# Kernel tuning notes

Hardware: AMD Instinct MI355X
Metric: run time of the kernel (lower is better)

## Reference

```python
import jax, jax.numpy as jnp
import numpy as np

K_MAX_X = 16
K_MAX_T = 16


def _k_actual(N, k_max):
    # low-mode indices [0..k_max] ++ [N-k_max..N-1], mapped to signed frequencies
    idx = np.concatenate([np.arange(k_max + 1), np.arange(N - k_max, N)]).astype(np.float32)
    return np.where(idx <= (N - 1) // 2, idx, idx - N)


def _phase(N, k_max, sign):
    # separable 1D truncated DFT factor: exp(sign*2*pi*i*k*n/N)/sqrt(N), shape [modes, N]
    k = _k_actual(N, k_max)
    n = np.arange(N, dtype=np.float32)
    ang = sign * 2.0 * np.pi * k[:, None] * n[None, :] / N
    return jnp.asarray((np.exp(1j * ang) / np.sqrt(N)).astype(np.complex64))


def setup_inputs() -> dict:
    key = jax.random.key(0)
    k1, k2, k3 = jax.random.split(key, 3)
    B, C_in, C_out, H, W = 16, 64, 64, 128, 128
    modes = 2 * K_MAX_X + 1  # 33
    scale = 1.0 / (C_in * C_out)
    x = jax.random.normal(k1, (B, C_in, H, W), dtype=jnp.float32)
    wr = scale * jax.random.uniform(k2, (C_in, C_out, modes, modes), dtype=jnp.float32)
    wi = scale * jax.random.uniform(k3, (C_in, C_out, modes, modes), dtype=jnp.float32)
    return {"x": x, "weights_real": wr, "weights_imag": wi}


def reference(x, weights_real, weights_imag):
    B, C, H, W = x.shape
    Px_f = _phase(H, K_MAX_X, -1.0)  # [mx, H]
    Pt_f = _phase(W, K_MAX_T, -1.0)  # [mt, W]
    Px_i = _phase(H, K_MAX_X, +1.0)
    Pt_i = _phase(W, K_MAX_T, +1.0)
    xc = x.astype(jnp.complex64)
    # truncated 2D DFT (separable): X[b,c,i,j]
    X = jnp.einsum('bcnm,in,jm->bcij', xc, Px_f, Pt_f)
    R = (weights_real + 1j * weights_imag).astype(jnp.complex64)
    out_kept = jnp.einsum('bcij,coij->boij', X, R)
    # truncated inverse DFT back to grid
    out = jnp.einsum('boij,in,jm->bonm', out_kept, Px_i, Pt_i)
    return jnp.real(out)
```

## Files before the change

### kernel.cpp

```cpp
#include <hip/hip_runtime.h>


#define NB   16
#define NC   64
#define NO   64
#define NH   128
#define NW   128
#define NM   33
#define WMODE (NM*NM)
#define MPAD  1092
#define NIMG 1024
#define NTOT (64*64*WMODE)
#define CPLANE (64*WMODE)

typedef __attribute__((ext_vector_type(8))) short s8v;
typedef __attribute__((ext_vector_type(4))) float f4v;

__device__ inline unsigned short f2bf(float f) {
  union { float f; unsigned u; } v; v.f = f;
  unsigned r = (v.u + 0x7FFFu + ((v.u >> 16) & 1u)) >> 16;
  return (unsigned short)r;
}

__device__ inline float bflo(unsigned u) {
  union { unsigned u; float f; } cv; cv.u = u << 16; return cv.f;
}
__device__ inline float bfhi(unsigned u) {
  union { unsigned u; float f; } cv; cv.u = u & 0xFFFF0000u; return cv.f;
}

__device__ inline s8v pack8(float4 a, float4 b) {
  s8v r;
  r[0] = (short)f2bf(a.x); r[1] = (short)f2bf(a.y);
  r[2] = (short)f2bf(a.z); r[3] = (short)f2bf(a.w);
  r[4] = (short)f2bf(b.x); r[5] = (short)f2bf(b.y);
  r[6] = (short)f2bf(b.z); r[7] = (short)f2bf(b.w);
  return r;
}

__device__ inline uint2 pack4(f4v a) {
  uint2 p;
  p.x = (unsigned)f2bf(a[0]) | ((unsigned)f2bf(a[1]) << 16);
  p.y = (unsigned)f2bf(a[2]) | ((unsigned)f2bf(a[3]) << 16);
  return p;
}

__device__ inline unsigned short phase_bf(int f, int x) {
  if (f >= 66) return 0;
  int g = (f < 33) ? f : f - 33;
  int fr = (g <= 16) ? g : g + 95;
  int ph = (fr * x) & 127;
  float ang = (float)ph * 0.04908738521234052f;
  float v = ((f < 33) ? cosf(ang) : sinf(ang)) * 0.08838834764831845f;
  return f2bf(v);
}

__global__ __launch_bounds__(256) void spc_tables(short* __restrict__ T1,
                                                  short* __restrict__ T2,
                                                  short* __restrict__ T3,
                                                  short* __restrict__ T4) {
  int tid = blockIdx.x * 256 + threadIdx.x;
  if (tid >= 49152) return;
  int f, x; short* dst;
  if (tid < 10240) {
    int e = tid & 7, l = (tid >> 3) & 63, q = tid >> 9;
    int ks = q / 5, jt = q - 5 * ks;
    f = jt * 16 + (l & 15); x = ks * 32 + (l >> 4) * 8 + e; dst = T1 + tid;
  } else if (tid < 20480) {
    int u = tid - 10240;
    int e = u & 7, l = (u >> 3) & 63, q = u >> 9;
    int it = q >> 2, ks = q & 3;
    f = it * 16 + (l & 15); x = ks * 32 + (l >> 4) * 8 + e; dst = T2 + u;
  } else if (tid < 36864) {
    int u = tid - 20480;
    int e = u & 7, l = (u >> 3) & 63, q = u >> 9;
    int cs = q >> 4, ks = (q >> 3) & 1, mt = q & 7;
    int j = ks * 32 + (l >> 4) * 8 + e;
    f = (j < 33) ? cs * 33 + j : 66;
    x = mt * 16 + (l & 15); dst = T3 + u;
  } else {
    int u = tid - 36864;
    int e = u & 7, l = (u >> 3) & 63, q = u >> 9;
    int nt = q / 3, ks = q - 3 * nt;
    int i2 = ks * 32 + (l >> 4) * 8 + e;
    if (i2 < 48) f = (i2 < 33) ? i2 : 66;
    else         f = (i2 - 48 < 33) ? 33 + (i2 - 48) : 66;
    x = nt * 16 + (l & 15); dst = T4 + u;
  }
  *dst = (short)phase_bf(f, x);
}

__global__ __launch_bounds__(256) void spc_wpack(const float* __restrict__ wr,
                                                 const float* __restrict__ wi,
                                                 unsigned* __restrict__ Wpk) {
  const int t = threadIdx.x;
  const size_t base = (size_t)blockIdx.x * 8192;
#pragma unroll 1
  for (int p = 0; p < 8; ++p) {
    const size_t L = base + (size_t)p * 1024 + (size_t)t * 4;
    if (L + 4 <= (size_t)NTOT) {
      float4 a = *reinterpret_cast<const float4*>(wr + L);
      float4 b = *reinterpret_cast<const float4*>(wi + L);
      float ae[4] = {a.x, a.y, a.z, a.w};
      float be[4] = {b.x, b.y, b.z, b.w};
#pragma unroll
      for (int e = 0; e < 4; ++e) {
        unsigned Li = (unsigned)L + e;
        unsigned c = Li / (unsigned)CPLANE;
        unsigned rem = Li - c * (unsigned)CPLANE;
        unsigned o = rem / (unsigned)WMODE;
        unsigned m = rem - o * (unsigned)WMODE;
        unsigned mch = m >> 6, ml = m & 63u;
        size_t D = ((((size_t)(o >> 1) * 18 + mch) * 64 + c) * 2 + (o & 1)) * 64 + ml;
        Wpk[D] = (unsigned)f2bf(ae[e]) | ((unsigned)f2bf(be[e]) << 16);
      }
    } else {
#pragma unroll
      for (int e = 0; e < 4; ++e) {
        size_t Li = L + e;
        if (Li < (size_t)NTOT) {
          unsigned Lu = (unsigned)Li;
          unsigned c = Lu / (unsigned)CPLANE;
          unsigned rem = Lu - c * (unsigned)CPLANE;
          unsigned o = rem / (unsigned)WMODE;
          unsigned m = rem - o * (unsigned)WMODE;
          unsigned mch = m >> 6, ml = m & 63u;
          size_t D = ((((size_t)(o >> 1) * 18 + mch) * 64 + c) * 2 + (o & 1)) * 64 + ml;
          Wpk[D] = (unsigned)f2bf(wr[Li]) | ((unsigned)f2bf(wi[Li]) << 16);
        }
      }
    }
  }
}

__global__ __launch_bounds__(256) void spc_fwd_mfma(const float* __restrict__ x,
                                                    const s8v* __restrict__ T1,
                                                    const s8v* __restrict__ T2,
                                                    unsigned* __restrict__ X2u) {
  __shared__ short Wt[80 * 128];
  __shared__ float Gs[80 * 84];
  const int t = threadIdx.x;
  const int l = t & 63;
  const int w = t >> 6;
  const int lr = l & 15;
  const int lg = l >> 4;
  const int img = blockIdx.x;
  const float* xp = x + (size_t)img * (NH * NW);

  for (int nn = 0; nn < 2; ++nn) {
    const int nt = 2 * w + nn;
    const float* xrow = xp + (nt * 16 + lr) * NW + lg * 8;
    s8v a[4];
#pragma unroll
    for (int ks = 0; ks < 4; ++ks) {
      float4 f0 = *reinterpret_cast<const float4*>(xrow + ks * 32);
      float4 f1 = *reinterpret_cast<const float4*>(xrow + ks * 32 + 4);
      a[ks] = pack8(f0, f1);
    }
#pragma unroll
    for (int jt = 0; jt < 5; ++jt) {
      f4v acc = {0.f, 0.f, 0.f, 0.f};
#pragma unroll
      for (int ks = 0; ks < 4; ++ks) {
        s8v b = T1[(ks * 5 + jt) * 64 + l];
        acc = __builtin_amdgcn_mfma_f32_16x16x32_bf16(a[ks], b, acc, 0, 0, 0);
      }
      int j = jt * 16 + lr;
      int g = ((nt * 16 + lg * 4) >> 2) ^ ((j & 7) << 2);
      *reinterpret_cast<uint2*>(&Wt[j * 128 + g * 4]) = pack4(acc);
    }
  }
  __syncthreads();

  for (int tix = w; tix < 25; tix += 4) {
    int it = tix / 5, j2 = tix - 5 * it;
    int jrow = j2 * 16 + lr;
    f4v acc = {0.f, 0.f, 0.f, 0.f};
#pragma unroll
    for (int ks = 0; ks < 4; ++ks) {
      s8v afr = T2[(it * 4 + ks) * 64 + l];
      int g = (ks * 8 + lg * 2) ^ ((jrow & 7) << 2);
      s8v b = *reinterpret_cast<const s8v*>(&Wt[jrow * 128 + g * 4]);
      acc = __builtin_amdgcn_mfma_f32_16x16x32_bf16(afr, b, acc, 0, 0, 0);
    }
    int gi = it * 16 + lg * 4;
#pragma unroll
    for (int r = 0; r < 4; ++r) Gs[(gi + r) * 84 + jrow] = acc[r];
  }
  __syncthreads();

  unsigned* X2p = X2u + (size_t)img * WMODE;
  for (int idx = t; idx < WMODE; idx += 256) {
    int i = idx / 33, j = idx - 33 * i;
    float g11 = Gs[i * 84 + j];
    float g22 = Gs[(i + 33) * 84 + (j + 33)];
    float g12 = Gs[i * 84 + (j + 33)];
    float g21 = Gs[(i + 33) * 84 + j];
    X2p[idx] = (unsigned)f2bf(g11 - g22) | ((unsigned)f2bf(-(g12 + g21)) << 16);
  }
}

__global__ __launch_bounds__(512) void spc_vmix(const unsigned* __restrict__ Wpk,
                                                const unsigned* __restrict__ X2u,
                                                short* __restrict__ Kbf) {
  __shared__ unsigned Ls[8192];
  const int t = threadIdx.x;
  const int ml = t & 63;
  const int w = t >> 6;
  const int b0 = w * 2;
  const int opair = blockIdx.x;
  const int mch = blockIdx.y;
  const int o0 = opair * 2;
  const int m = mch * 64 + ml;
  const int mc = (m > 1088) ? 1088 : m;

  {
    const uint4* src = reinterpret_cast<const uint4*>(
        Wpk + ((size_t)opair * 18 + mch) * 8192);
    uint4* dst = reinterpret_cast<uint4*>(Ls);
#pragma unroll
    for (int p = 0; p < 4; ++p) dst[p * 512 + t] = src[p * 512 + t];
  }
  __syncthreads();

  const unsigned* xp = X2u + (size_t)(b0 * 64) * WMODE + mc;

  float aR[2][2], aI[2][2];
#pragma unroll
  for (int j = 0; j < 2; ++j)
#pragma unroll
    for (int oo = 0; oo < 2; ++oo) { aR[j][oo] = 0.f; aI[j][oo] = 0.f; }

#pragma unroll 1
  for (int c4 = 0; c4 < 16; ++c4) {
    unsigned u[4][2];
#pragma unroll
    for (int q = 0; q < 4; ++q) {
      const int c = c4 * 4 + q;
#pragma unroll
      for (int j = 0; j < 2; ++j)
        u[q][j] = xp[(size_t)(j * 64 + c) * WMODE];
    }
#pragma unroll
    for (int q = 0; q < 4; ++q) {
      const int c = c4 * 4 + q;
      const unsigned w0 = Ls[(c * 2 + 0) * 64 + ml];
      const unsigned w1 = Ls[(c * 2 + 1) * 64 + ml];
      const float wr0 = bflo(w0), wi0 = bfhi(w0);
      const float wr1 = bflo(w1), wi1 = bfhi(w1);
#pragma unroll
      for (int j = 0; j < 2; ++j) {
        const float xr_ = bflo(u[q][j]);
        const float xi_ = bfhi(u[q][j]);
        aR[j][0] = fmaf(xr_, wr0, fmaf(-xi_, wi0, aR[j][0]));
        aI[j][0] = fmaf(xr_, wi0, fmaf( xi_, wr0, aI[j][0]));
        aR[j][1] = fmaf(xr_, wr1, fmaf(-xi_, wi1, aR[j][1]));
        aI[j][1] = fmaf(xr_, wi1, fmaf( xi_, wr1, aI[j][1]));
      }
    }
  }

  if (m < WMODE) {
#pragma unroll
    for (int j = 0; j < 2; ++j)
#pragma unroll
      for (int oo = 0; oo < 2; ++oo) {
        size_t img = (size_t)(b0 + j) * 64 + o0 + oo;
        Kbf[img * (2 * MPAD) + m]        = (short)f2bf(aR[j][oo]);
        Kbf[img * (2 * MPAD) + MPAD + m] = (short)f2bf(aI[j][oo]);
      }
  }
}

__global__ __launch_bounds__(256) void spc_inv_mfma(const short* __restrict__ Kbf,
                                                    const s8v* __restrict__ T3,
                                                    const s8v* __restrict__ T4,
                                                    float* __restrict__ out) {
  __shared__ short Kls2[2 * MPAD];
  __shared__ short Vt[128 * 128];
  const int t = threadIdx.x;
  const int l = t & 63;
  const int w = t >> 6;
  const int lr = l & 15;
  const int lg = l >> 4;
  const int img = blockIdx.x;

  {
    const uint4* src = reinterpret_cast<const uint4*>(Kbf + (size_t)img * (2 * MPAD));
    uint4* dstl = reinterpret_cast<uint4*>(Kls2);
    for (int idx = t; idx < 273; idx += 256) dstl[idx] = src[idx];
  }
  __syncthreads();

  s8v fr[2][3][2];
#pragma unroll
  for (int ri2 = 0; ri2 < 2; ++ri2)
#pragma unroll
    for (int it = 0; it < 3; ++it)
#pragma unroll
      for (int ks = 0; ks < 2; ++ks) {
        const int i = it * 16 + lr;
#pragma unroll
        for (int e = 0; e < 8; ++e) {
          const int j = ks * 32 + lg * 8 + e;
          unsigned short v = (i < 33 && j < 33)
              ? (unsigned short)Kls2[ri2 * MPAD + i * 33 + j] : (unsigned short)0;
          fr[ri2][it][ks][e] = (short)v;
        }
      }

  for (int mm = 0; mm < 2; ++mm) {
    const int mt = w * 2 + mm;
    const int m = mt * 16 + lr;
    s8v cw[2], sw[2], nsw[2];
#pragma unroll
    for (int ks = 0; ks < 2; ++ks) {
      cw[ks] = T3[((0 * 2 + ks) * 8 + mt) * 64 + l];
      sw[ks] = T3[((1 * 2 + ks) * 8 + mt) * 64 + l];
#pragma unroll
      for (int e = 0; e < 8; ++e)
        nsw[ks][e] = (short)(((unsigned short)sw[ks][e]) ^ 0x8000u);
    }
#pragma unroll
    for (int it = 0; it < 3; ++it) {
      f4v t1 = {0.f, 0.f, 0.f, 0.f}, t2 = {0.f, 0.f, 0.f, 0.f};
#pragma unroll
      for (int ks = 0; ks < 2; ++ks) {
        t1 = __builtin_amdgcn_mfma_f32_16x16x32_bf16(fr[0][it][ks], cw[ks],  t1, 0, 0, 0);
        t1 = __builtin_amdgcn_mfma_f32_16x16x32_bf16(fr[1][it][ks], nsw[ks], t1, 0, 0, 0);
        t2 = __builtin_amdgcn_mfma_f32_16x16x32_bf16(fr[1][it][ks], cw[ks],  t2, 0, 0, 0);
        t2 = __builtin_amdgcn_mfma_f32_16x16x32_bf16(fr[0][it][ks], sw[ks],  t2, 0, 0, 0);
      }
      const int base1 = it * 16 + lg * 4;
      const int g1 = (base1 >> 2) ^ ((m & 7) << 2);
      *reinterpret_cast<uint2*>(&Vt[m * 128 + g1 * 4]) = pack4(t1);
      f4v nt2v = {-t2[0], -t2[1], -t2[2], -t2[3]};
      const int g2 = ((48 + base1) >> 2) ^ ((m & 7) << 2);
      *reinterpret_cast<uint2*>(&Vt[m * 128 + g2 * 4]) = pack4(nt2v);
    }
  }
  __syncthreads();

  float* op = out + (size_t)img * (NH * NW);
  for (int nn = 0; nn < 2; ++nn) {
    const int nt = w * 2 + nn;
    s8v a[3];
#pragma unroll
    for (int ks = 0; ks < 3; ++ks) a[ks] = T4[(nt * 3 + ks) * 64 + l];
    for (int mt = 0; mt < 8; ++mt) {
      const int m = mt * 16 + lr;
      f4v acc = {0.f, 0.f, 0.f, 0.f};
#pragma unroll
      for (int ks = 0; ks < 3; ++ks) {
        const int g = (ks * 8 + lg * 2) ^ ((m & 7) << 2);
        s8v bb = *reinterpret_cast<const s8v*>(&Vt[m * 128 + g * 4]);
        acc = __builtin_amdgcn_mfma_f32_16x16x32_bf16(a[ks], bb, acc, 0, 0, 0);
      }
      const int n = nt * 16 + lg * 4;
#pragma unroll
      for (int r = 0; r < 4; ++r) op[(n + r) * NW + m] = acc[r];
    }
  }
}

extern "C" void kernel_launch(void* const* d_in, const int* in_sizes, int n_in,
                              void* d_out, int out_size, void* d_ws, size_t ws_size,
                              hipStream_t stream) {
  const float* x  = (const float*)d_in[0];
  const float* wr = (const float*)d_in[1];
  const float* wi = (const float*)d_in[2];
  float* out = (float*)d_out;

  char* ws = (char*)d_ws;
  short* T1 = (short*)(ws);
  short* T2 = (short*)(ws + 20480);
  short* T3 = (short*)(ws + 40960);
  short* T4 = (short*)(ws + 73728);
  unsigned* X2u = (unsigned*)(ws + 98304);
  short* Kbf = (short*)(ws + 4558848);
  unsigned* Wpk = (unsigned*)(ws + 9031680);

  hipLaunchKernelGGL(spc_tables, dim3(192), dim3(256), 0, stream, T1, T2, T3, T4);
  hipLaunchKernelGGL(spc_wpack, dim3(545), dim3(256), 0, stream, wr, wi, Wpk);
  hipLaunchKernelGGL(spc_fwd_mfma, dim3(NIMG), dim3(256), 0, stream,
                     x, (const s8v*)T1, (const s8v*)T2, X2u);
  hipLaunchKernelGGL(spc_vmix, dim3(32, 18), dim3(512), 0, stream,
                     Wpk, X2u, Kbf);
  hipLaunchKernelGGL(spc_inv_mfma, dim3(NIMG), dim3(256), 0, stream,
                     Kbf, (const s8v*)T3, (const s8v*)T4, out);
}
```

Baseline: 76.06 us.

## Repack spectral activations mode-major and retile channel mixing into 16-mode groups

Adds a transpose kernel that repacks the forward-spectrum activations from [b,c,mode] into a mode-major [mode,c,b] buffer. The mixing kernel is retiled to 16-mode groups per block with both activations and weights staged in shared memory, so each thread forms one (b,o,mode) dot product over channels. Results are staged in shared memory before being written out. The weight packing is reordered to match. The aim is to replace strided global loads of activations with coalesced, reused shared-memory tiles, at the cost of an extra launch and an extra pass over the activation buffer.

After: 90.11 us. +18.5%, slower.

```diff
diff --git a/kernel.cpp b/kernel.cpp
--- a/kernel.cpp
+++ b/kernel.cpp
@@ -9,9 +9,10 @@
 #define NM   33
 #define WMODE (NM*NM)
 #define MPAD  1092
+#define XPM   1104
+#define MG    69
 #define NIMG 1024
 #define NTOT (64*64*WMODE)
-#define CPLANE (64*WMODE)
 
 typedef __attribute__((ext_vector_type(8))) short s8v;
 typedef __attribute__((ext_vector_type(4))) float f4v;
@@ -94,9 +95,9 @@
                                                  const float* __restrict__ wi,
                                                  unsigned* __restrict__ Wpk) {
   const int t = threadIdx.x;
-  const size_t base = (size_t)blockIdx.x * 8192;
+  const size_t base = (size_t)blockIdx.x * 4096;
 #pragma unroll 1
-  for (int p = 0; p < 8; ++p) {
+  for (int p = 0; p < 4; ++p) {
     const size_t L = base + (size_t)p * 1024 + (size_t)t * 4;
     if (L + 4 <= (size_t)NTOT) {
       float4 a = *reinterpret_cast<const float4*>(wr + L);
@@ -106,12 +107,10 @@
 #pragma unroll
       for (int e = 0; e < 4; ++e) {
         unsigned Li = (unsigned)L + e;
-        unsigned c = Li / (unsigned)CPLANE;
-        unsigned rem = Li - c * (unsigned)CPLANE;
-        unsigned o = rem / (unsigned)WMODE;
-        unsigned m = rem - o * (unsigned)WMODE;
-        unsigned mch = m >> 6, ml = m & 63u;
-        size_t D = ((((size_t)(o >> 1) * 18 + mch) * 64 + c) * 2 + (o & 1)) * 64 + ml;
+        unsigned co = Li / (unsigned)WMODE;
+        unsigned m  = Li - co * (unsigned)WMODE;
+        unsigned c = co >> 6, o = co & 63u;
+        size_t D = ((((size_t)(o >> 1) * MG + (m >> 4)) * 64 + c) * 2 + (o & 1)) * 16 + (m & 15);
         Wpk[D] = (unsigned)f2bf(ae[e]) | ((unsigned)f2bf(be[e]) << 16);
       }
     } else {
@@ -120,12 +119,10 @@
         size_t Li = L + e;
         if (Li < (size_t)NTOT) {
           unsigned Lu = (unsigned)Li;
-          unsigned c = Lu / (unsigned)CPLANE;
-          unsigned rem = Lu - c * (unsigned)CPLANE;
-          unsigned o = rem / (unsigned)WMODE;
-          unsigned m = rem - o * (unsigned)WMODE;
-          unsigned mch = m >> 6, ml = m & 63u;
-          size_t D = ((((size_t)(o >> 1) * 18 + mch) * 64 + c) * 2 + (o & 1)) * 64 + ml;
+          unsigned co = Lu / (unsigned)WMODE;
+          unsigned m  = Lu - co * (unsigned)WMODE;
+          unsigned c = co >> 6, o = co & 63u;
+          size_t D = ((((size_t)(o >> 1) * MG + (m >> 4)) * 64 + c) * 2 + (o & 1)) * 16 + (m & 15);
           Wpk[D] = (unsigned)f2bf(wr[Li]) | ((unsigned)f2bf(wi[Li]) << 16);
         }
       }
@@ -200,75 +197,97 @@
   }
 }
 
+__global__ __launch_bounds__(256) void spc_xrepack(const unsigned* __restrict__ X2u,
+                                                   unsigned* __restrict__ Xp) {
+  __shared__ unsigned Ls[32 * 65];
+  const int t = threadIdx.x;
+  const int l = t & 63;
+  const int w = t >> 6;
+  const int m0 = blockIdx.x * 64;
+  const int c0 = blockIdx.y * 2;
+
+  {
+    unsigned vv[8];
+    const int m = m0 + l;
+#pragma unroll
+    for (int rr = 0; rr < 8; ++rr) {
+      int r = w * 8 + rr;
+      int b = r & 15, cl = r >> 4;
+      vv[rr] = (m < WMODE) ? X2u[(size_t)(b * 64 + c0 + cl) * WMODE + m] : 0u;
+    }
+#pragma unroll
+    for (int rr = 0; rr < 8; ++rr)
+      Ls[(w * 8 + rr) * 65 + l] = vv[rr];
+  }
+  __syncthreads();
+  for (int p = 0; p < 8; ++p) {
+    int m_l = p * 8 + w * 2 + (l >> 5);
+    int m = m0 + m_l;
+    if (m >= XPM) continue;
+    int cl = (l >> 4) & 1, b = l & 15;
+    unsigned v = Ls[(cl * 16 + b) * 65 + m_l];
+    Xp[((size_t)m * 64 + c0 + cl) * 16 + b] = v;
+  }
+}
+
 __global__ __launch_bounds__(512) void spc_vmix(const unsigned* __restrict__ Wpk,
-                                                const unsigned* __restrict__ X2u,
+                                                const unsigned* __restrict__ Xp,
                                                 short* __restrict__ Kbf) {
-  __shared__ unsigned Ls[8192];
+  __shared__ unsigned Xl[16 * 1028];
+  __shared__ unsigned Wl[2048];
+  __shared__ unsigned short Ols[1024];
   const int t = threadIdx.x;
-  const int ml = t & 63;
+  const int l = t & 63;
   const int w = t >> 6;
-  const int b0 = w * 2;
   const int opair = blockIdx.x;
-  const int mch = blockIdx.y;
-  const int o0 = opair * 2;
-  const int m = mch * 64 + ml;
-  const int mc = (m > 1088) ? 1088 : m;
+  const int mg = blockIdx.y;
+  const int m0 = mg * 16;
 
   {
+    const uint4* src = reinterpret_cast<const uint4*>(Xp + (size_t)m0 * 1024);
+#pragma unroll
+    for (int p = 0; p < 8; ++p) {
+      int idx = p * 512 + t;
+      int row = idx >> 8, col = idx & 255;
+      *reinterpret_cast<uint4*>(&Xl[row * 1028 + col * 4]) = src[idx];
+    }
+  }
+  if (t < 512) {
     const uint4* src = reinterpret_cast<const uint4*>(
-        Wpk + ((size_t)opair * 18 + mch) * 8192);
-    uint4* dst = reinterpret_cast<uint4*>(Ls);
-#pragma unroll
-    for (int p = 0; p < 4; ++p) dst[p * 512 + t] = src[p * 512 + t];
-  }
-  __syncthreads();
-
-  const unsigned* xp = X2u + (size_t)(b0 * 64) * WMODE + mc;
-
-  float aR[2][2], aI[2][2];
-#pragma unroll
-  for (int j = 0; j < 2; ++j)
-#pragma unroll
-    for (int oo = 0; oo < 2; ++oo) { aR[j][oo] = 0.f; aI[j][oo] = 0.f; }
-
-#pragma unroll 1
-  for (int c4 = 0; c4 < 16; ++c4) {
-    unsigned u[4][2];
-#pragma unroll
-    for (int q = 0; q < 4; ++q) {
-      const int c = c4 * 4 + q;
-#pragma unroll
-      for (int j = 0; j < 2; ++j)
-        u[q][j] = xp[(size_t)(j * 64 + c) * WMODE];
-    }
-#pragma unroll
-    for (int q = 0; q < 4; ++q) {
-      const int c = c4 * 4 + q;
-      const unsigned w0 = Ls[(c * 2 + 0) * 64 + ml];
-      const unsigned w1 = Ls[(c * 2 + 1) * 64 + ml];
-      const float wr0 = bflo(w0), wi0 = bfhi(w0);
-      const float wr1 = bflo(w1), wi1 = bfhi(w1);
-#pragma unroll
-      for (int j = 0; j < 2; ++j) {
-        const float xr_ = bflo(u[q][j]);
-        const float xi_ = bfhi(u[q][j]);
-        aR[j][0] = fmaf(xr_, wr0, fmaf(-xi_, wi0, aR[j][0]));
-        aI[j][0] = fmaf(xr_, wi0, fmaf( xi_, wr0, aI[j][0]));
-        aR[j][1] = fmaf(xr_, wr1, fmaf(-xi_, wi1, aR[j][1]));
-        aI[j][1] = fmaf(xr_, wi1, fmaf( xi_, wr1, aI[j][1]));
-      }
-    }
-  }
-
-  if (m < WMODE) {
-#pragma unroll
-    for (int j = 0; j < 2; ++j)
-#pragma unroll
-      for (int oo = 0; oo < 2; ++oo) {
-        size_t img = (size_t)(b0 + j) * 64 + o0 + oo;
-        Kbf[img * (2 * MPAD) + m]        = (short)f2bf(aR[j][oo]);
-        Kbf[img * (2 * MPAD) + MPAD + m] = (short)f2bf(aI[j][oo]);
-      }
+        Wpk + ((size_t)opair * MG + mg) * 2048);
+    *reinterpret_cast<uint4*>(&Wl[t * 4]) = src[t];
+  }
+  __syncthreads();
+
+  const int bg = w >> 1, oo = w & 1;
+  const int m_l = l >> 2, bl = l & 3;
+  const int xbase = m_l * 1028 + bg * 4 + bl;
+  const int wbase = oo * 16 + m_l;
+
+  float aR = 0.f, aI = 0.f;
+#pragma unroll 4
+  for (int c = 0; c < 64; ++c) {
+    unsigned xv = Xl[xbase + c * 16];
+    unsigned wv = Wl[wbase + c * 32];
+    float xr = bflo(xv), xi = bfhi(xv);
+    float wre = bflo(wv), wim = bfhi(wv);
+    aR = fmaf(xr, wre, fmaf(-xi, wim, aR));
+    aI = fmaf(xr, wim, fmaf( xi, wre, aI));
+  }
+
+  const int b = bg * 4 + bl;
+  Ols[((oo * 16 + b) * 2 + 0) * 16 + m_l] = f2bf(aR);
+  Ols[((oo * 16 + b) * 2 + 1) * 16 + m_l] = f2bf(aI);
+  __syncthreads();
+
+  if (t < 256) {
+    const int pair = t >> 2, q = t & 3;
+    if (!(mg == 68 && q > 0)) {
+      const int oo2 = pair >> 5, b2 = (pair >> 1) & 15, ri = pair & 1;
+      const size_t img = (size_t)b2 * 64 + opair * 2 + oo2;
+      uint2 v = *reinterpret_cast<const uint2*>(&Ols[pair * 16 + q * 4]);
+      *reinterpret_cast<uint2*>(Kbf + img * (2 * MPAD) + (size_t)ri * MPAD + m0 + q * 4) = v;
+    }
   }
 }
 
@@ -378,14 +397,16 @@
   short* T4 = (short*)(ws + 73728);
   unsigned* X2u = (unsigned*)(ws + 98304);
   short* Kbf = (short*)(ws + 4558848);
-  unsigned* Wpk = (unsigned*)(ws + 9031680);
+  unsigned* Xp = (unsigned*)(ws + 9031680);
+  unsigned* Wpk = (unsigned*)(ws + 13553664);
 
   hipLaunchKernelGGL(spc_tables, dim3(192), dim3(256), 0, stream, T1, T2, T3, T4);
-  hipLaunchKernelGGL(spc_wpack, dim3(545), dim3(256), 0, stream, wr, wi, Wpk);
+  hipLaunchKernelGGL(spc_wpack, dim3(1090), dim3(256), 0, stream, wr, wi, Wpk);
   hipLaunchKernelGGL(spc_fwd_mfma, dim3(NIMG), dim3(256), 0, stream,
                      x, (const s8v*)T1, (const s8v*)T2, X2u);
-  hipLaunchKernelGGL(spc_vmix, dim3(32, 18), dim3(512), 0, stream,
-                     Wpk, X2u, Kbf);
+  hipLaunchKernelGGL(spc_xrepack, dim3(18, 32), dim3(256), 0, stream, X2u, Xp);
+  hipLaunchKernelGGL(spc_vmix, dim3(32, MG), dim3(512), 0, stream,
+                     Wpk, Xp, Kbf);
   hipLaunchKernelGGL(spc_inv_mfma, dim3(NIMG), dim3(256), 0, stream,
                      Kbf, (const s8v*)T3, (const s8v*)T4, out);
 }
```
